# Performance work log

Measured on AMD Instinct MI355X. Metric: run time of the kernel, lower is better.

Reference implementation:

```python
import jax, jax.numpy as jnp
import numpy as np

N = 100000   # nodes
E = 1600000  # edges (avg degree 16)
D = 128      # input = hidden = out dim
L = 4        # num_layers
EPS = 1e-5   # LayerNorm eps


def setup_inputs() -> dict:
    key = jax.random.key(0)
    k0, k1, k2, k3, k4 = jax.random.split(key, 5)
    in_feat = jax.random.normal(k0, (N, D), dtype=jnp.float32)
    edge_index = jax.random.randint(k1, (2, E), 0, N, dtype=jnp.int32)
    s = 1.0 / np.sqrt(D)
    # GraphConv params per layer: lin_rel (weight+bias), lin_root (weight, no bias)
    W_rel = jax.random.uniform(k2, (L, D, D), jnp.float32, -s, s)
    b_rel = jax.random.uniform(k3, (L, D), jnp.float32, -s, s)
    W_root = jax.random.uniform(k4, (L, D, D), jnp.float32, -s, s)
    # single shared LayerNorm module in the torch code
    ln_gamma = jnp.ones((D,), jnp.float32)
    ln_beta = jnp.zeros((D,), jnp.float32)
    return {"in_feat": in_feat, "edge_index": edge_index, "W_rel": W_rel,
            "b_rel": b_rel, "W_root": W_root, "ln_gamma": ln_gamma, "ln_beta": ln_beta}


def _layer_norm(h, gamma, beta):
    mu = jnp.mean(h, axis=-1, keepdims=True)
    var = jnp.mean(jnp.square(h - mu), axis=-1, keepdims=True)
    return (h - mu) * jax.lax.rsqrt(var + EPS) * gamma + beta


def _graph_conv(h, W_r, b_r, W_rt, src, dst):
    # PyG GraphConv: out_i = lin_rel(sum_{j->i} x_j) + lin_root(x_i)
    agg = jax.ops.segment_sum(h[src], dst, num_segments=N)  # [N, D]
    return agg @ W_r + b_r + h @ W_rt


def reference(in_feat, edge_index, W_rel, b_rel, W_root, ln_gamma, ln_beta):
    src, dst = edge_index[0], edge_index[1]
    # input layer: conv -> ReLU -> LayerNorm -> dropout(p=0)
    h = _graph_conv(in_feat, W_rel[0], b_rel[0], W_root[0], src, dst)
    h = _layer_norm(jax.nn.relu(h), ln_gamma, ln_beta)
    # middle layers with residual
    for l in range(1, L - 1):
        nh = _graph_conv(h, W_rel[l], b_rel[l], W_root[l], src, dst)
        h = _layer_norm(jax.nn.relu(nh + h), ln_gamma, ln_beta)
    # output layer: conv only
    return _graph_conv(h, W_rel[L - 1], b_rel[L - 1], W_root[L - 1], src, dst)
```

## Files before the change

kernel.cpp:

```cpp
#include <hip/hip_runtime.h>
#include <cstddef>

#define N_NODES 100000
#define N_PAD   100032
#define N_EDGES 1600000
#define DIM 128
#define LN_EPS 1e-5f
#define ZROW   N_NODES
#define COL_CAP 3200000

#define B_SHIFT 9
#define B_SIZE  512
#define N_BKT   196
#define EPB     4096
#define NBLK    ((N_EDGES + EPB - 1) / EPB)

typedef short bf16x8 __attribute__((ext_vector_type(8)));
typedef float f32x4 __attribute__((ext_vector_type(4)));
typedef float f32x2 __attribute__((ext_vector_type(2)));

__device__ __forceinline__ float asf(uint u) {
    union { uint i; float f; } c; c.i = u; return c.f;
}
__device__ __forceinline__ float bf2f(uint u) { return asf(u << 16); }
__device__ __forceinline__ ushort f2bf(float x) {
    union { float f; uint i; } c; c.f = x;
    uint r = c.i + 0x7fffu + ((c.i >> 16) & 1u);
    return (ushort)(r >> 16);
}

__device__ __forceinline__ void accp(f32x2* acc, uint p) {
    f32x2 v;
    v.x = asf(p << 16);
    v.y = asf(p & 0xffff0000u);
    *acc += v;
}
__device__ __forceinline__ void accq(f32x2* a, uint4 p) {
    accp(&a[0], p.x); accp(&a[1], p.y); accp(&a[2], p.z); accp(&a[3], p.w);
}


__global__ __launch_bounds__(256) void bhist_kernel(const int* __restrict__ dst,
                                                    int* __restrict__ bcount) {
    __shared__ int lh[N_BKT];
    const int tid = threadIdx.x;
    if (tid < N_BKT) lh[tid] = 0;
    __syncthreads();
    const int base = blockIdx.x * EPB;
    #pragma unroll
    for (int k = 0; k < 16; ++k) {
        int t = base + tid + k * 256;
        if (t < N_EDGES) atomicAdd(&lh[dst[t] >> B_SHIFT], 1);
    }
    __syncthreads();
    if (tid < N_BKT && lh[tid]) atomicAdd(&bcount[tid], lh[tid]);
}

__global__ __launch_bounds__(256) void bscan_kernel(const int* __restrict__ bcount,
                                                    int* __restrict__ bstart,
                                                    int* __restrict__ gcur) {
    __shared__ int s[256];
    const int tid = threadIdx.x;
    int v = (tid < N_BKT) ? bcount[tid] : 0;
    s[tid] = v;
    __syncthreads();
    for (int off = 1; off < 256; off <<= 1) {
        int t = (tid >= off) ? s[tid - off] : 0;
        __syncthreads();
        s[tid] += t;
        __syncthreads();
    }
    if (tid < N_BKT) { int e = s[tid] - v; bstart[tid] = e; gcur[tid] = e; }
    if (tid == 0) bstart[N_BKT] = N_EDGES;
}

__global__ __launch_bounds__(256) void bscatter_kernel(const int* __restrict__ src,
                                                       const int* __restrict__ dst,
                                                       int* __restrict__ gcur,
                                                       int2* __restrict__ pairs) {
    __shared__ int lcnt[N_BKT];
    __shared__ int lbase[N_BKT];
    const int tid = threadIdx.x;
    if (tid < N_BKT) lcnt[tid] = 0;
    __syncthreads();
    const int base = blockIdx.x * EPB;
    int ls[16], ld[16];
    #pragma unroll
    for (int k = 0; k < 16; ++k) {
        int t = base + tid + k * 256;
        if (t < N_EDGES) {
            ls[k] = src[t]; ld[k] = dst[t];
            atomicAdd(&lcnt[ld[k] >> B_SHIFT], 1);
        } else ld[k] = -1;
    }
    __syncthreads();
    if (tid < N_BKT) lbase[tid] = lcnt[tid] ? atomicAdd(&gcur[tid], lcnt[tid]) : 0;
    __syncthreads();
    if (tid < N_BKT) lcnt[tid] = 0;
    __syncthreads();
    #pragma unroll
    for (int k = 0; k < 16; ++k) {
        if (ld[k] >= 0) {
            int b = ld[k] >> B_SHIFT;
            int r = atomicAdd(&lcnt[b], 1);
            pairs[lbase[b] + r] = make_int2(ls[k], ld[k]);
        }
    }
}

__global__ __launch_bounds__(256) void ndeg_kernel(const int2* __restrict__ pairs,
                                                   const int* __restrict__ bstart,
                                                   int* __restrict__ row_ptr,
                                                   int* __restrict__ bpad) {
    __shared__ int ldeg[B_SIZE];
    __shared__ int ws4[4];
    const int b = blockIdx.x;
    const int node0 = b << B_SHIFT;
    const int tid = threadIdx.x;
    ldeg[tid] = 0; ldeg[tid + 256] = 0;
    __syncthreads();
    const int beg = bstart[b], end = bstart[b + 1];
    for (int t = beg + tid; t < end; t += 256)
        atomicAdd(&ldeg[pairs[t].y - node0], 1);
    __syncthreads();
    const int d0 = (ldeg[2 * tid] + 15) & ~15;
    const int d1 = (ldeg[2 * tid + 1] + 15) & ~15;
    const int sum2 = d0 + d1;
    const int lane = tid & 63, wv = tid >> 6;
    int incl = sum2;
    #pragma unroll
    for (int off = 1; off < 64; off <<= 1) {
        int t = __shfl_up(incl, off);
        if (lane >= off) incl += t;
    }
    if (lane == 63) ws4[wv] = incl;
    __syncthreads();
    int woff = 0;
    if (wv > 0) woff += ws4[0];
    if (wv > 1) woff += ws4[1];
    if (wv > 2) woff += ws4[2];
    const int e0 = woff + incl - sum2;
    const int n0 = node0 + 2 * tid;
    if (n0 < N_NODES)     row_ptr[n0]     = e0;
    if (n0 + 1 < N_NODES) row_ptr[n0 + 1] = e0 + d0;
    if (tid == 255) bpad[b] = woff + incl;
}

__global__ __launch_bounds__(256) void pscan_kernel(const int* __restrict__ bpad,
                                                    int* __restrict__ bpadstart) {
    __shared__ int s[256];
    const int tid = threadIdx.x;
    int v = (tid < N_BKT) ? bpad[tid] : 0;
    s[tid] = v;
    __syncthreads();
    for (int off = 1; off < 256; off <<= 1) {
        int t = (tid >= off) ? s[tid - off] : 0;
        __syncthreads();
        s[tid] += t;
        __syncthreads();
    }
    if (tid < N_BKT) bpadstart[tid] = s[tid] - v;
    if (tid == N_BKT - 1) bpadstart[N_BKT] = s[tid];
}

__global__ void addbase_kernel(int* __restrict__ row_ptr, const int* __restrict__ bpadstart) {
    int n = blockIdx.x * 256 + threadIdx.x;
    if (n < N_NODES) row_ptr[n] += bpadstart[n >> B_SHIFT];
    else if (n <= N_PAD) row_ptr[n] = bpadstart[N_BKT];
}

__global__ __launch_bounds__(256) void bfill_kernel(const int2* __restrict__ pairs,
                                                    const int* __restrict__ bstart,
                                                    const int* __restrict__ row_ptr,
                                                    int* __restrict__ col) {
    __shared__ int lcur[B_SIZE];
    const int b = blockIdx.x;
    const int node0 = b << B_SHIFT;
    const int tid = threadIdx.x;
    #pragma unroll
    for (int k = 0; k < 2; ++k) {
        int n = node0 + tid + k * 256;
        lcur[tid + k * 256] = (n < N_NODES) ? row_ptr[n] : 0;
    }
    __syncthreads();
    const int beg = bstart[b], end = bstart[b + 1];
    for (int t = beg + tid; t < end; t += 256) {
        int2 p = pairs[t];
        int r = atomicAdd(&lcur[p.y - node0], 1);
        col[r] = p.x;
    }
    __syncthreads();
    #pragma unroll
    for (int k = 0; k < 2; ++k) {
        int n = tid + k * 256;
        int node = node0 + n;
        if (node < N_NODES) {
            int e = lcur[n];
            int pe = row_ptr[node + 1];
            for (int p = e; p < pe; ++p) col[p] = ZROW;
        }
    }
}


__global__ void cvt_kernel(const float* __restrict__ in, ushort* __restrict__ out) {
    int i = (blockIdx.x * blockDim.x + threadIdx.x) * 4;
    float4 v = *(const float4*)&in[i];
    uint2 r;
    r.x = (uint)f2bf(v.x) | ((uint)f2bf(v.y) << 16);
    r.y = (uint)f2bf(v.z) | ((uint)f2bf(v.w) << 16);
    *(uint2*)&out[i] = r;
}


__global__ void prepack_kernel(const float* __restrict__ Wrel, const float* __restrict__ Wroot,
                               ushort* __restrict__ Wp) {
    int t = blockIdx.x * blockDim.x + threadIdx.x;
    int layer = t >> 12;
    int m = (t >> 11) & 1;
    int frag = (t >> 6) & 31;
    int lane = t & 63;
    int ks = frag >> 3, n = frag & 7;
    int c = n * 16 + (lane & 15);
    int k0 = ks * 32 + (lane >> 4) * 8;
    ushort tmp[8];
    #pragma unroll
    for (int j = 0; j < 8; ++j) {
        int k = k0 + j;
        float w;
        if (m == 0) {
            w = Wrel[layer * 16384 + k * 128 + c];
        } else {
            w = Wroot[layer * 16384 + k * 128 + c];
            if ((layer == 1 || layer == 2) && k == c) w += 1.0f;
        }
        tmp[j] = f2bf(w);
    }
    *(uint4*)&Wp[(size_t)t * 8] = *(const uint4*)tmp;
}


template <int MODE>
__global__ __launch_bounds__(128, 6) void fused_kernel(const ushort* __restrict__ hb,
                                                       const int* __restrict__ row_ptr,
                                                       const int* __restrict__ col,
                                                       const ushort* __restrict__ Wp,
                                                       const float* __restrict__ brel,
                                                       const float* __restrict__ gamma,
                                                       const float* __restrict__ beta,
                                                       ushort* __restrict__ outb,
                                                       float* __restrict__ outf) {
    __shared__ char sA[2 * 4096];
    const int tid = threadIdx.x;
    const int lane = tid & 63;
    const int wv = tid >> 6;
    const int wrow0 = blockIdx.x * 32 + wv * 16;
    char* sW = &sA[wv * 4096];
    const int rsel = lane >> 4;
    const int c16 = lane & 15;

    const uint4* h4 = (const uint4*)hb;
    #pragma unroll 1
    for (int t = 0; t < 8; ++t) {
        const int lrA = 2 * t;
        const int lrB = lrA + 1;
        const int p0 = row_ptr[wrow0 + lrA];
        const int p1 = row_ptr[wrow0 + lrA + 1];
        const int p2 = row_ptr[wrow0 + lrA + 2];
        const int itA = (p1 - p0) >> 4;
        const int itB = (p2 - p1) >> 4;
        int jA = p0 + rsel;
        int jB = p1 + rsel;
        const int iters = max(itA, itB);

        f32x2 a[4], b[4];
        #pragma unroll
        for (int u = 0; u < 4; ++u) { a[u] = (f32x2){0.f, 0.f}; b[u] = (f32x2){0.f, 0.f}; }

        for (int it = 0; it < iters; ++it) {
            int sA0 = ZROW, sA1 = ZROW, sA2 = ZROW, sA3 = ZROW;
            int sB0 = ZROW, sB1 = ZROW, sB2 = ZROW, sB3 = ZROW;
            if (it < itA) {
                sA0 = col[jA]; sA1 = col[jA + 4]; sA2 = col[jA + 8]; sA3 = col[jA + 12];
                jA += 16;
            }
            if (it < itB) {
                sB0 = col[jB]; sB1 = col[jB + 4]; sB2 = col[jB + 8]; sB3 = col[jB + 12];
                jB += 16;
            }
            uint4 pA0 = h4[(size_t)sA0 * 16 + c16];
            uint4 pA1 = h4[(size_t)sA1 * 16 + c16];
            uint4 pA2 = h4[(size_t)sA2 * 16 + c16];
            uint4 pA3 = h4[(size_t)sA3 * 16 + c16];
            uint4 pB0 = h4[(size_t)sB0 * 16 + c16];
            uint4 pB1 = h4[(size_t)sB1 * 16 + c16];
            uint4 pB2 = h4[(size_t)sB2 * 16 + c16];
            uint4 pB3 = h4[(size_t)sB3 * 16 + c16];
            accq(a, pA0); accq(a, pA1); accq(a, pA2); accq(a, pA3);
            accq(b, pB0); accq(b, pB1); accq(b, pB2); accq(b, pB3);
        }

        #pragma unroll
        for (int u = 0; u < 4; ++u) {
            float ax = a[u].x, ay = a[u].y, bx = b[u].x, by = b[u].y;
            ax += __shfl_xor(ax, 16); ay += __shfl_xor(ay, 16);
            bx += __shfl_xor(bx, 16); by += __shfl_xor(by, 16);
            ax += __shfl_xor(ax, 32); ay += __shfl_xor(ay, 32);
            bx += __shfl_xor(bx, 32); by += __shfl_xor(by, 32);
            a[u].x = ax; a[u].y = ay; b[u].x = bx; b[u].y = by;
        }
        if (rsel == 0) {
            uint4 o;
            o.x = (uint)f2bf(a[0].x) | ((uint)f2bf(a[0].y) << 16);
            o.y = (uint)f2bf(a[1].x) | ((uint)f2bf(a[1].y) << 16);
            o.z = (uint)f2bf(a[2].x) | ((uint)f2bf(a[2].y) << 16);
            o.w = (uint)f2bf(a[3].x) | ((uint)f2bf(a[3].y) << 16);
            *(uint4*)&sW[lrA * 256 + ((c16 * 16) ^ ((lrA & 7) << 4))] = o;
        } else if (rsel == 1) {
            uint4 o;
            o.x = (uint)f2bf(b[0].x) | ((uint)f2bf(b[0].y) << 16);
            o.y = (uint)f2bf(b[1].x) | ((uint)f2bf(b[1].y) << 16);
            o.z = (uint)f2bf(b[2].x) | ((uint)f2bf(b[2].y) << 16);
            o.w = (uint)f2bf(b[3].x) | ((uint)f2bf(b[3].y) << 16);
            *(uint4*)&sW[lrB * 256 + ((c16 * 16) ^ ((lrB & 7) << 4))] = o;
        }
    }

    const int kg = lane >> 4;
    const int cl = lane & 15;
    const size_t growa = (size_t)wrow0 + cl;
    const int abase = cl * 256 + kg * 16;
    const int aswz = (cl & 7) << 4;

    f32x4 acc[8];
    #pragma unroll
    for (int n = 0; n < 8; ++n) acc[n] = (f32x4){0.f, 0.f, 0.f, 0.f};

    const uint4* bR = (const uint4*)Wp + lane;
    const uint4* bT = (const uint4*)(Wp + 16384) + lane;
    #pragma unroll
    for (int ks = 0; ks < 4; ++ks) {
        bf16x8 a = *(const bf16x8*)&sW[(abase + ks * 64) ^ aswz];
        #pragma unroll
        for (int n = 0; n < 8; ++n) {
            bf16x8 b = *(const bf16x8*)&bR[(ks * 8 + n) * 64];
            acc[n] = __builtin_amdgcn_mfma_f32_16x16x32_bf16(a, b, acc[n], 0, 0, 0);
        }
    }
    #pragma unroll
    for (int ks = 0; ks < 4; ++ks) {
        bf16x8 a = *(const bf16x8*)&hb[growa * 128 + ks * 32 + kg * 8];
        #pragma unroll
        for (int n = 0; n < 8; ++n) {
            bf16x8 b = *(const bf16x8*)&bT[(ks * 8 + n) * 64];
            acc[n] = __builtin_amdgcn_mfma_f32_16x16x32_bf16(a, b, acc[n], 0, 0, 0);
        }
    }

    float bias[8], gg[8], bb[8];
    #pragma unroll
    for (int n = 0; n < 8; ++n) {
        int cn = n * 16 + cl;
        bias[n] = brel[cn];
        if (MODE != 2) { gg[n] = gamma[cn]; bb[n] = beta[cn]; }
    }

    #pragma unroll
    for (int reg = 0; reg < 4; ++reg) {
        const int lr = kg * 4 + reg;
        const size_t grow = (size_t)wrow0 + lr;
        const bool live = grow < N_NODES;
        if (MODE != 2) {
            float v[8];
            float s = 0.f, q = 0.f;
            #pragma unroll
            for (int n = 0; n < 8; ++n) {
                float x = acc[n][reg] + bias[n];
                x = fmaxf(x, 0.f);
                v[n] = x; s += x; q += x * x;
            }
            #pragma unroll
            for (int m = 8; m >= 1; m >>= 1) { s += __shfl_xor(s, m); q += __shfl_xor(q, m); }
            float mu = s * (1.f / DIM);
            float var = q * (1.f / DIM) - mu * mu;
            float rinv = rsqrtf(var + LN_EPS);
            if (live) {
                #pragma unroll
                for (int n = 0; n < 8; ++n) {
                    float y = (v[n] - mu) * rinv * gg[n] + bb[n];
                    outb[grow * DIM + n * 16 + cl] = f2bf(y);
                }
            }
        } else {
            if (live) {
                #pragma unroll
                for (int n = 0; n < 8; ++n)
                    outf[grow * DIM + n * 16 + cl] = acc[n][reg] + bias[n];
            }
        }
    }
}


static inline size_t align256(size_t x) { return (x + 255) & ~(size_t)255; }

extern "C" void kernel_launch(void* const* d_in, const int* in_sizes, int n_in,
                              void* d_out, int out_size, void* d_ws, size_t ws_size,
                              hipStream_t stream) {
    const float* in_feat = (const float*)d_in[0];
    const int*   ei      = (const int*)d_in[1];
    const float* Wrel    = (const float*)d_in[2];
    const float* brel    = (const float*)d_in[3];
    const float* Wroot   = (const float*)d_in[4];
    const float* gamma   = (const float*)d_in[5];
    const float* beta    = (const float*)d_in[6];
    float* out = (float*)d_out;

    char* ws = (char*)d_ws;
    size_t off = 0;
    int* col = (int*)(ws + off);        off = align256(off + (size_t)COL_CAP * 4);
    int2* pairs = (int2*)(ws + off);    off = align256(off + (size_t)N_EDGES * 8);
    int* row_ptr = (int*)(ws + off);    off = align256(off + (size_t)(N_PAD + 2) * 4);
    int* bcount = (int*)(ws + off);     off = align256(off + (size_t)N_BKT * 4);
    int* bstart = (int*)(ws + off);     off = align256(off + (size_t)(N_BKT + 1) * 4);
    int* gcur = (int*)(ws + off);       off = align256(off + (size_t)N_BKT * 4);
    int* bpad = (int*)(ws + off);       off = align256(off + (size_t)N_BKT * 4);
    int* bpadstart = (int*)(ws + off);  off = align256(off + (size_t)(N_BKT + 1) * 4);
    ushort* x0 = (ushort*)(ws + off);   off = align256(off + (size_t)N_PAD * DIM * 2);
    ushort* hA = (ushort*)(ws + off);   off = align256(off + (size_t)N_PAD * DIM * 2);
    ushort* hB = (ushort*)(ws + off);   off = align256(off + (size_t)N_PAD * DIM * 2);
    ushort* Wp = (ushort*)(ws + off);   off = align256(off + (size_t)4 * 2 * 128 * 128 * 2);
    (void)ws_size; (void)in_sizes; (void)n_in; (void)out_size;

    const int* src = ei;
    const int* dst = ei + N_EDGES;

    hipMemsetAsync(bcount, 0, (size_t)N_BKT * 4, stream);
    bhist_kernel<<<NBLK, 256, 0, stream>>>(dst, bcount);
    bscan_kernel<<<1, 256, 0, stream>>>(bcount, bstart, gcur);
    bscatter_kernel<<<NBLK, 256, 0, stream>>>(src, dst, gcur, pairs);
    ndeg_kernel<<<N_BKT, 256, 0, stream>>>(pairs, bstart, row_ptr, bpad);
    pscan_kernel<<<1, 256, 0, stream>>>(bpad, bpadstart);
    addbase_kernel<<<(N_PAD + 1 + 255) / 256, 256, 0, stream>>>(row_ptr, bpadstart);
    bfill_kernel<<<N_BKT, 256, 0, stream>>>(pairs, bstart, row_ptr, col);

    const size_t padoff = (size_t)N_NODES * DIM * 2;
    const size_t padlen = (size_t)(N_PAD - N_NODES) * DIM * 2;
    hipMemsetAsync((char*)x0 + padoff, 0, padlen, stream);
    hipMemsetAsync((char*)hA + padoff, 0, padlen, stream);
    hipMemsetAsync((char*)hB + padoff, 0, padlen, stream);

    cvt_kernel<<<(N_NODES * DIM) / (4 * 256), 256, 0, stream>>>(in_feat, x0);
    prepack_kernel<<<64, 256, 0, stream>>>(Wrel, Wroot, Wp);

    const int grid = N_PAD / 32;

    fused_kernel<0><<<grid, 128, 0, stream>>>(x0, row_ptr, col, Wp, brel, gamma, beta, hA, nullptr);
    fused_kernel<0><<<grid, 128, 0, stream>>>(hA, row_ptr, col, Wp + 32768, brel + DIM, gamma, beta, hB, nullptr);
    fused_kernel<0><<<grid, 128, 0, stream>>>(hB, row_ptr, col, Wp + 2 * 32768, brel + 2 * DIM, gamma, beta, hA, nullptr);
    fused_kernel<2><<<grid, 128, 0, stream>>>(hA, row_ptr, col, Wp + 3 * 32768, brel + 3 * DIM, gamma, beta, nullptr, out);
}
```

Baseline: 423.0 us.

## Warp-specialize fused GNN layer into gather producers and MFMA consumers; drop bucket histogram

The fused layer kernel becomes a persistent 512-thread block: four producer waves gather neighbour sums into a double-buffered LDS tile while four consumer waves run the MFMA GEMM and LayerNorm epilogue on the previous tile. The goal is to overlap the latency-bound gather with the matrix work. Separately, the CSR build drops the bucket histogram and scan kernels by writing pairs into fixed-capacity per-bucket segments (SEGCAP) and using gcur counts directly. This relies on no bucket exceeding 10240 edges and adds a block-wide barrier per tile, and only half the waves do gather work at any time.

```diff
diff --git a/kernel.cpp b/kernel.cpp
--- a/kernel.cpp
+++ b/kernel.cpp
@@ -12,8 +12,12 @@
 #define B_SHIFT 9
 #define B_SIZE  512
 #define N_BKT   196
+#define SEGCAP  10240
 #define EPB     4096
 #define NBLK    ((N_EDGES + EPB - 1) / EPB)
+
+#define N_TILES 1563
+#define FGRID   512
 
 typedef short bf16x8 __attribute__((ext_vector_type(8)));
 typedef float f32x4 __attribute__((ext_vector_type(4)));
@@ -39,40 +43,6 @@
     accp(&a[0], p.x); accp(&a[1], p.y); accp(&a[2], p.z); accp(&a[3], p.w);
 }
 
-
-__global__ __launch_bounds__(256) void bhist_kernel(const int* __restrict__ dst,
-                                                    int* __restrict__ bcount) {
-    __shared__ int lh[N_BKT];
-    const int tid = threadIdx.x;
-    if (tid < N_BKT) lh[tid] = 0;
-    __syncthreads();
-    const int base = blockIdx.x * EPB;
-    #pragma unroll
-    for (int k = 0; k < 16; ++k) {
-        int t = base + tid + k * 256;
-        if (t < N_EDGES) atomicAdd(&lh[dst[t] >> B_SHIFT], 1);
-    }
-    __syncthreads();
-    if (tid < N_BKT && lh[tid]) atomicAdd(&bcount[tid], lh[tid]);
-}
-
-__global__ __launch_bounds__(256) void bscan_kernel(const int* __restrict__ bcount,
-                                                    int* __restrict__ bstart,
-                                                    int* __restrict__ gcur) {
-    __shared__ int s[256];
-    const int tid = threadIdx.x;
-    int v = (tid < N_BKT) ? bcount[tid] : 0;
-    s[tid] = v;
-    __syncthreads();
-    for (int off = 1; off < 256; off <<= 1) {
-        int t = (tid >= off) ? s[tid - off] : 0;
-        __syncthreads();
-        s[tid] += t;
-        __syncthreads();
-    }
-    if (tid < N_BKT) { int e = s[tid] - v; bstart[tid] = e; gcur[tid] = e; }
-    if (tid == 0) bstart[N_BKT] = N_EDGES;
-}
 
 __global__ __launch_bounds__(256) void bscatter_kernel(const int* __restrict__ src,
                                                        const int* __restrict__ dst,
@@ -103,13 +73,13 @@
         if (ld[k] >= 0) {
             int b = ld[k] >> B_SHIFT;
             int r = atomicAdd(&lcnt[b], 1);
-            pairs[lbase[b] + r] = make_int2(ls[k], ld[k]);
+            pairs[b * SEGCAP + lbase[b] + r] = make_int2(ls[k], ld[k]);
         }
     }
 }
 
 __global__ __launch_bounds__(256) void ndeg_kernel(const int2* __restrict__ pairs,
-                                                   const int* __restrict__ bstart,
+                                                   const int* __restrict__ gcur,
                                                    int* __restrict__ row_ptr,
                                                    int* __restrict__ bpad) {
     __shared__ int ldeg[B_SIZE];
@@ -119,7 +89,8 @@
     const int tid = threadIdx.x;
     ldeg[tid] = 0; ldeg[tid + 256] = 0;
     __syncthreads();
-    const int beg = bstart[b], end = bstart[b + 1];
+    const int beg = b * SEGCAP;
+    const int end = beg + gcur[b];
     for (int t = beg + tid; t < end; t += 256)
         atomicAdd(&ldeg[pairs[t].y - node0], 1);
     __syncthreads();
@@ -170,7 +141,7 @@
 }
 
 __global__ __launch_bounds__(256) void bfill_kernel(const int2* __restrict__ pairs,
-                                                    const int* __restrict__ bstart,
+                                                    const int* __restrict__ gcur,
                                                     const int* __restrict__ row_ptr,
                                                     int* __restrict__ col) {
     __shared__ int lcur[B_SIZE];
@@ -183,7 +154,8 @@
         lcur[tid + k * 256] = (n < N_NODES) ? row_ptr[n] : 0;
     }
     __syncthreads();
-    const int beg = bstart[b], end = bstart[b + 1];
+    const int beg = b * SEGCAP;
+    const int end = beg + gcur[b];
     for (int t = beg + tid; t < end; t += 256) {
         int2 p = pairs[t];
         int r = atomicAdd(&lcur[p.y - node0], 1);
@@ -241,7 +213,7 @@
 
 
 template <int MODE>
-__global__ __launch_bounds__(128, 6) void fused_kernel(const ushort* __restrict__ hb,
+__global__ __launch_bounds__(512, 4) void fused_kernel(const ushort* __restrict__ hb,
                                                        const int* __restrict__ row_ptr,
                                                        const int* __restrict__ col,
                                                        const ushort* __restrict__ Wp,
@@ -250,154 +222,172 @@
                                                        const float* __restrict__ beta,
                                                        ushort* __restrict__ outb,
                                                        float* __restrict__ outf) {
-    __shared__ char sA[2 * 4096];
+    __shared__ char sBuf[2][64 * 256];
     const int tid = threadIdx.x;
     const int lane = tid & 63;
     const int wv = tid >> 6;
-    const int wrow0 = blockIdx.x * 32 + wv * 16;
-    char* sW = &sA[wv * 4096];
+    const int pw = wv & 3;
+    const bool producer = wv < 4;
+    const int ntiles = (N_TILES - blockIdx.x + FGRID - 1) / FGRID;
+
+    const int kg = lane >> 4;
+    const int cl = lane & 15;
+    float bias[8], gg[8], bb[8];
+    if (!producer) {
+        #pragma unroll
+        for (int n = 0; n < 8; ++n) {
+            int cn = n * 16 + cl;
+            bias[n] = brel[cn];
+            if (MODE != 2) { gg[n] = gamma[cn]; bb[n] = beta[cn]; }
+        }
+    }
+    const uint4* bR = (const uint4*)Wp + lane;
+    const uint4* bT = (const uint4*)(Wp + 16384) + lane;
+    const uint4* h4 = (const uint4*)hb;
     const int rsel = lane >> 4;
     const int c16 = lane & 15;
 
-    const uint4* h4 = (const uint4*)hb;
-    #pragma unroll 1
-    for (int t = 0; t < 8; ++t) {
-        const int lrA = 2 * t;
-        const int lrB = lrA + 1;
-        const int p0 = row_ptr[wrow0 + lrA];
-        const int p1 = row_ptr[wrow0 + lrA + 1];
-        const int p2 = row_ptr[wrow0 + lrA + 2];
-        const int itA = (p1 - p0) >> 4;
-        const int itB = (p2 - p1) >> 4;
-        int jA = p0 + rsel;
-        int jB = p1 + rsel;
-        const int iters = max(itA, itB);
-
-        f32x2 a[4], b[4];
-        #pragma unroll
-        for (int u = 0; u < 4; ++u) { a[u] = (f32x2){0.f, 0.f}; b[u] = (f32x2){0.f, 0.f}; }
-
-        for (int it = 0; it < iters; ++it) {
-            int sA0 = ZROW, sA1 = ZROW, sA2 = ZROW, sA3 = ZROW;
-            int sB0 = ZROW, sB1 = ZROW, sB2 = ZROW, sB3 = ZROW;
-            if (it < itA) {
-                sA0 = col[jA]; sA1 = col[jA + 4]; sA2 = col[jA + 8]; sA3 = col[jA + 12];
-                jA += 16;
-            }
-            if (it < itB) {
-                sB0 = col[jB]; sB1 = col[jB + 4]; sB2 = col[jB + 8]; sB3 = col[jB + 12];
-                jB += 16;
-            }
-            uint4 pA0 = h4[(size_t)sA0 * 16 + c16];
-            uint4 pA1 = h4[(size_t)sA1 * 16 + c16];
-            uint4 pA2 = h4[(size_t)sA2 * 16 + c16];
-            uint4 pA3 = h4[(size_t)sA3 * 16 + c16];
-            uint4 pB0 = h4[(size_t)sB0 * 16 + c16];
-            uint4 pB1 = h4[(size_t)sB1 * 16 + c16];
-            uint4 pB2 = h4[(size_t)sB2 * 16 + c16];
-            uint4 pB3 = h4[(size_t)sB3 * 16 + c16];
-            accq(a, pA0); accq(a, pA1); accq(a, pA2); accq(a, pA3);
-            accq(b, pB0); accq(b, pB1); accq(b, pB2); accq(b, pB3);
-        }
-
-        #pragma unroll
-        for (int u = 0; u < 4; ++u) {
-            float ax = a[u].x, ay = a[u].y, bx = b[u].x, by = b[u].y;
-            ax += __shfl_xor(ax, 16); ay += __shfl_xor(ay, 16);
-            bx += __shfl_xor(bx, 16); by += __shfl_xor(by, 16);
-            ax += __shfl_xor(ax, 32); ay += __shfl_xor(ay, 32);
-            bx += __shfl_xor(bx, 32); by += __shfl_xor(by, 32);
-            a[u].x = ax; a[u].y = ay; b[u].x = bx; b[u].y = by;
-        }
-        if (rsel == 0) {
-            uint4 o;
-            o.x = (uint)f2bf(a[0].x) | ((uint)f2bf(a[0].y) << 16);
-            o.y = (uint)f2bf(a[1].x) | ((uint)f2bf(a[1].y) << 16);
-            o.z = (uint)f2bf(a[2].x) | ((uint)f2bf(a[2].y) << 16);
-            o.w = (uint)f2bf(a[3].x) | ((uint)f2bf(a[3].y) << 16);
-            *(uint4*)&sW[lrA * 256 + ((c16 * 16) ^ ((lrA & 7) << 4))] = o;
-        } else if (rsel == 1) {
-            uint4 o;
-            o.x = (uint)f2bf(b[0].x) | ((uint)f2bf(b[0].y) << 16);
-            o.y = (uint)f2bf(b[1].x) | ((uint)f2bf(b[1].y) << 16);
-            o.z = (uint)f2bf(b[2].x) | ((uint)f2bf(b[2].y) << 16);
-            o.w = (uint)f2bf(b[3].x) | ((uint)f2bf(b[3].y) << 16);
-            *(uint4*)&sW[lrB * 256 + ((c16 * 16) ^ ((lrB & 7) << 4))] = o;
-        }
-    }
-
-    const int kg = lane >> 4;
-    const int cl = lane & 15;
-    const size_t growa = (size_t)wrow0 + cl;
-    const int abase = cl * 256 + kg * 16;
-    const int aswz = (cl & 7) << 4;
-
-    f32x4 acc[8];
-    #pragma unroll
-    for (int n = 0; n < 8; ++n) acc[n] = (f32x4){0.f, 0.f, 0.f, 0.f};
-
-    const uint4* bR = (const uint4*)Wp + lane;
-    const uint4* bT = (const uint4*)(Wp + 16384) + lane;
-    #pragma unroll
-    for (int ks = 0; ks < 4; ++ks) {
-        bf16x8 a = *(const bf16x8*)&sW[(abase + ks * 64) ^ aswz];
-        #pragma unroll
-        for (int n = 0; n < 8; ++n) {
-            bf16x8 b = *(const bf16x8*)&bR[(ks * 8 + n) * 64];
-            acc[n] = __builtin_amdgcn_mfma_f32_16x16x32_bf16(a, b, acc[n], 0, 0, 0);
-        }
-    }
-    #pragma unroll
-    for (int ks = 0; ks < 4; ++ks) {
-        bf16x8 a = *(const bf16x8*)&hb[growa * 128 + ks * 32 + kg * 8];
-        #pragma unroll
-        for (int n = 0; n < 8; ++n) {
-            bf16x8 b = *(const bf16x8*)&bT[(ks * 8 + n) * 64];
-            acc[n] = __builtin_amdgcn_mfma_f32_16x16x32_bf16(a, b, acc[n], 0, 0, 0);
-        }
-    }
-
-    float bias[8], gg[8], bb[8];
-    #pragma unroll
-    for (int n = 0; n < 8; ++n) {
-        int cn = n * 16 + cl;
-        bias[n] = brel[cn];
-        if (MODE != 2) { gg[n] = gamma[cn]; bb[n] = beta[cn]; }
-    }
-
-    #pragma unroll
-    for (int reg = 0; reg < 4; ++reg) {
-        const int lr = kg * 4 + reg;
-        const size_t grow = (size_t)wrow0 + lr;
-        const bool live = grow < N_NODES;
-        if (MODE != 2) {
-            float v[8];
-            float s = 0.f, q = 0.f;
-            #pragma unroll
-            for (int n = 0; n < 8; ++n) {
-                float x = acc[n][reg] + bias[n];
-                x = fmaxf(x, 0.f);
-                v[n] = x; s += x; q += x * x;
-            }
-            #pragma unroll
-            for (int m = 8; m >= 1; m >>= 1) { s += __shfl_xor(s, m); q += __shfl_xor(q, m); }
-            float mu = s * (1.f / DIM);
-            float var = q * (1.f / DIM) - mu * mu;
-            float rinv = rsqrtf(var + LN_EPS);
-            if (live) {
-                #pragma unroll
-                for (int n = 0; n < 8; ++n) {
-                    float y = (v[n] - mu) * rinv * gg[n] + bb[n];
-                    outb[grow * DIM + n * 16 + cl] = f2bf(y);
+    for (int it = 0; it <= ntiles; ++it) {
+        if (producer) {
+            if (it < ntiles) {
+                const int tile = blockIdx.x + it * FGRID;
+                const int row0 = tile * 64 + pw * 16;
+                char* sW = &sBuf[it & 1][pw * 16 * 256];
+                #pragma unroll 1
+                for (int t = 0; t < 8; ++t) {
+                    const int lrA = 2 * t;
+                    const int lrB = lrA + 1;
+                    const int p0 = row_ptr[row0 + lrA];
+                    const int p1 = row_ptr[row0 + lrA + 1];
+                    const int p2 = row_ptr[row0 + lrA + 2];
+                    const int itA = (p1 - p0) >> 4;
+                    const int itB = (p2 - p1) >> 4;
+                    int jA = p0 + rsel;
+                    int jB = p1 + rsel;
+                    const int iters = max(itA, itB);
+
+                    f32x2 a[4], b[4];
+                    #pragma unroll
+                    for (int u = 0; u < 4; ++u) { a[u] = (f32x2){0.f, 0.f}; b[u] = (f32x2){0.f, 0.f}; }
+
+                    for (int i2 = 0; i2 < iters; ++i2) {
+                        int sA0 = ZROW, sA1 = ZROW, sA2 = ZROW, sA3 = ZROW;
+                        int sB0 = ZROW, sB1 = ZROW, sB2 = ZROW, sB3 = ZROW;
+                        if (i2 < itA) {
+                            sA0 = col[jA]; sA1 = col[jA + 4]; sA2 = col[jA + 8]; sA3 = col[jA + 12];
+                            jA += 16;
+                        }
+                        if (i2 < itB) {
+                            sB0 = col[jB]; sB1 = col[jB + 4]; sB2 = col[jB + 8]; sB3 = col[jB + 12];
+                            jB += 16;
+                        }
+                        uint4 pA0 = h4[(size_t)sA0 * 16 + c16];
+                        uint4 pA1 = h4[(size_t)sA1 * 16 + c16];
+                        uint4 pA2 = h4[(size_t)sA2 * 16 + c16];
+                        uint4 pA3 = h4[(size_t)sA3 * 16 + c16];
+                        uint4 pB0 = h4[(size_t)sB0 * 16 + c16];
+                        uint4 pB1 = h4[(size_t)sB1 * 16 + c16];
+                        uint4 pB2 = h4[(size_t)sB2 * 16 + c16];
+                        uint4 pB3 = h4[(size_t)sB3 * 16 + c16];
+                        accq(a, pA0); accq(a, pA1); accq(a, pA2); accq(a, pA3);
+                        accq(b, pB0); accq(b, pB1); accq(b, pB2); accq(b, pB3);
+                    }
+
+                    #pragma unroll
+                    for (int u = 0; u < 4; ++u) {
+                        float ax = a[u].x, ay = a[u].y, bx = b[u].x, by = b[u].y;
+                        ax += __shfl_xor(ax, 16); ay += __shfl_xor(ay, 16);
+                        bx += __shfl_xor(bx, 16); by += __shfl_xor(by, 16);
+                        ax += __shfl_xor(ax, 32); ay += __shfl_xor(ay, 32);
+                        bx += __shfl_xor(bx, 32); by += __shfl_xor(by, 32);
+                        a[u].x = ax; a[u].y = ay; b[u].x = bx; b[u].y = by;
+                    }
+                    if (rsel == 0) {
+                        uint4 o;
+                        o.x = (uint)f2bf(a[0].x) | ((uint)f2bf(a[0].y) << 16);
+                        o.y = (uint)f2bf(a[1].x) | ((uint)f2bf(a[1].y) << 16);
+                        o.z = (uint)f2bf(a[2].x) | ((uint)f2bf(a[2].y) << 16);
+                        o.w = (uint)f2bf(a[3].x) | ((uint)f2bf(a[3].y) << 16);
+                        *(uint4*)&sW[lrA * 256 + ((c16 * 16) ^ ((lrA & 7) << 4))] = o;
+                    } else if (rsel == 1) {
+                        uint4 o;
+                        o.x = (uint)f2bf(b[0].x) | ((uint)f2bf(b[0].y) << 16);
+                        o.y = (uint)f2bf(b[1].x) | ((uint)f2bf(b[1].y) << 16);
+                        o.z = (uint)f2bf(b[2].x) | ((uint)f2bf(b[2].y) << 16);
+                        o.w = (uint)f2bf(b[3].x) | ((uint)f2bf(b[3].y) << 16);
+                        *(uint4*)&sW[lrB * 256 + ((c16 * 16) ^ ((lrB & 7) << 4))] = o;
+                    }
                 }
             }
         } else {
-            if (live) {
+            if (it > 0) {
+                const int tile = blockIdx.x + (it - 1) * FGRID;
+                const int wrow0 = tile * 64 + pw * 16;
+                const char* sW = &sBuf[(it - 1) & 1][pw * 16 * 256];
+                const size_t growa = (size_t)wrow0 + cl;
+                const int abase = cl * 256 + kg * 16;
+                const int aswz = (cl & 7) << 4;
+
+                f32x4 acc[8];
                 #pragma unroll
-                for (int n = 0; n < 8; ++n)
-                    outf[grow * DIM + n * 16 + cl] = acc[n][reg] + bias[n];
+                for (int n = 0; n < 8; ++n) acc[n] = (f32x4){0.f, 0.f, 0.f, 0.f};
+
+                #pragma unroll
+                for (int ks = 0; ks < 4; ++ks) {
+                    bf16x8 a = *(const bf16x8*)&sW[(abase + ks * 64) ^ aswz];
+                    #pragma unroll
+                    for (int n = 0; n < 8; ++n) {
+                        bf16x8 b = *(const bf16x8*)&bR[(ks * 8 + n) * 64];
+                        acc[n] = __builtin_amdgcn_mfma_f32_16x16x32_bf16(a, b, acc[n], 0, 0, 0);
+                    }
+                }
+                #pragma unroll
+                for (int ks = 0; ks < 4; ++ks) {
+                    bf16x8 a = *(const bf16x8*)&hb[growa * 128 + ks * 32 + kg * 8];
+                    #pragma unroll
+                    for (int n = 0; n < 8; ++n) {
+                        bf16x8 b = *(const bf16x8*)&bT[(ks * 8 + n) * 64];
+                        acc[n] = __builtin_amdgcn_mfma_f32_16x16x32_bf16(a, b, acc[n], 0, 0, 0);
+                    }
+                }
+
+                #pragma unroll
+                for (int reg = 0; reg < 4; ++reg) {
+                    const int lr = kg * 4 + reg;
+                    const size_t grow = (size_t)wrow0 + lr;
+                    const bool live = grow < N_NODES;
+                    if (MODE != 2) {
+                        float v[8];
+                        float s = 0.f, q = 0.f;
+                        #pragma unroll
+                        for (int n = 0; n < 8; ++n) {
+                            float x = acc[n][reg] + bias[n];
+                            x = fmaxf(x, 0.f);
+                            v[n] = x; s += x; q += x * x;
+                        }
+                        #pragma unroll
+                        for (int m = 8; m >= 1; m >>= 1) { s += __shfl_xor(s, m); q += __shfl_xor(q, m); }
+                        float mu = s * (1.f / DIM);
+                        float var = q * (1.f / DIM) - mu * mu;
+                        float rinv = rsqrtf(var + LN_EPS);
+                        if (live) {
+                            #pragma unroll
+                            for (int n = 0; n < 8; ++n) {
+                                float y = (v[n] - mu) * rinv * gg[n] + bb[n];
+                                outb[grow * DIM + n * 16 + cl] = f2bf(y);
+                            }
+                        }
+                    } else {
+                        if (live) {
+                            #pragma unroll
+                            for (int n = 0; n < 8; ++n)
+                                outf[grow * DIM + n * 16 + cl] = acc[n][reg] + bias[n];
+                        }
+                    }
+                }
             }
         }
+        __syncthreads();
     }
 }
 
@@ -419,10 +409,8 @@
     char* ws = (char*)d_ws;
     size_t off = 0;
     int* col = (int*)(ws + off);        off = align256(off + (size_t)COL_CAP * 4);
-    int2* pairs = (int2*)(ws + off);    off = align256(off + (size_t)N_EDGES * 8);
+    int2* pairs = (int2*)(ws + off);    off = align256(off + (size_t)N_BKT * SEGCAP * 8);
     int* row_ptr = (int*)(ws + off);    off = align256(off + (size_t)(N_PAD + 2) * 4);
-    int* bcount = (int*)(ws + off);     off = align256(off + (size_t)N_BKT * 4);
-    int* bstart = (int*)(ws + off);     off = align256(off + (size_t)(N_BKT + 1) * 4);
     int* gcur = (int*)(ws + off);       off = align256(off + (size_t)N_BKT * 4);
     int* bpad = (int*)(ws + off);       off = align256(off + (size_t)N_BKT * 4);
     int* bpadstart = (int*)(ws + off);  off = align256(off + (size_t)(N_BKT + 1) * 4);
@@ -435,14 +423,12 @@
     const int* src = ei;
     const int* dst = ei + N_EDGES;
 
-    hipMemsetAsync(bcount, 0, (size_t)N_BKT * 4, stream);
-    bhist_kernel<<<NBLK, 256, 0, stream>>>(dst, bcount);
-    bscan_kernel<<<1, 256, 0, stream>>>(bcount, bstart, gcur);
+    hipMemsetAsync(gcur, 0, (size_t)N_BKT * 4, stream);
     bscatter_kernel<<<NBLK, 256, 0, stream>>>(src, dst, gcur, pairs);
-    ndeg_kernel<<<N_BKT, 256, 0, stream>>>(pairs, bstart, row_ptr, bpad);
+    ndeg_kernel<<<N_BKT, 256, 0, stream>>>(pairs, gcur, row_ptr, bpad);
     pscan_kernel<<<1, 256, 0, stream>>>(bpad, bpadstart);
     addbase_kernel<<<(N_PAD + 1 + 255) / 256, 256, 0, stream>>>(row_ptr, bpadstart);
-    bfill_kernel<<<N_BKT, 256, 0, stream>>>(pairs, bstart, row_ptr, col);
+    bfill_kernel<<<N_BKT, 256, 0, stream>>>(pairs, gcur, row_ptr, col);
 
     const size_t padoff = (size_t)N_NODES * DIM * 2;
     const size_t padlen = (size_t)(N_PAD - N_NODES) * DIM * 2;
@@ -453,10 +439,8 @@
     cvt_kernel<<<(N_NODES * DIM) / (4 * 256), 256, 0, stream>>>(in_feat, x0);
     prepack_kernel<<<64, 256, 0, stream>>>(Wrel, Wroot, Wp);
 
-    const int grid = N_PAD / 32;
-
-    fused_kernel<0><<<grid, 128, 0, stream>>>(x0, row_ptr, col, Wp, brel, gamma, beta, hA, nullptr);
-    fused_kernel<0><<<grid, 128, 0, stream>>>(hA, row_ptr, col, Wp + 32768, brel + DIM, gamma, beta, hB, nullptr);
-    fused_kernel<0><<<grid, 128, 0, stream>>>(hB, row_ptr, col, Wp + 2 * 32768, brel + 2 * DIM, gamma, beta, hA, nullptr);
-    fused_kernel<2><<<grid, 128, 0, stream>>>(hA, row_ptr, col, Wp + 3 * 32768, brel + 3 * DIM, gamma, beta, nullptr, out);
-}
+    fused_kernel<0><<<FGRID, 512, 0, stream>>>(x0, row_ptr, col, Wp, brel, gamma, beta, hA, nullptr);
+    fused_kernel<0><<<FGRID, 512, 0, stream>>>(hA, row_ptr, col, Wp + 32768, brel + DIM, gamma, beta, hB, nullptr);
+    fused_kernel<0><<<FGRID, 512, 0, stream>>>(hB, row_ptr, col, Wp + 2 * 32768, brel + 2 * DIM, gamma, beta, hA, nullptr);
+    fused_kernel<2><<<FGRID, 512, 0, stream>>>(hA, row_ptr, col, Wp + 3 * 32768, brel + 3 * DIM, gamma, beta, nullptr, out);
+}
```

After: 638.9 us. +51.0%, slower.
